# Kernel tuning notes

Hardware: AMD Instinct MI355X
Metric: run time of the kernel (lower is better)

The kernel has to match this reference:

```python
import jax, jax.numpy as jnp
import numpy as np

N_EMBD = 1024
N_HEAD = 16
MASK_FILL = -10000.0


def setup_inputs() -> dict:
    key = jax.random.key(0)
    ks = jax.random.split(key, 9)
    s = 1.0 / np.sqrt(N_EMBD)
    d = {"x": jax.random.normal(ks[0], (4, 2048, N_EMBD), dtype=jnp.float32)}
    for i, name in enumerate(["k", "q", "v", "p"]):
        d[f"W{name}"] = jax.random.uniform(ks[1 + 2 * i], (N_EMBD, N_EMBD), minval=-s, maxval=s, dtype=jnp.float32)
        d[f"b{name}"] = jax.random.uniform(ks[2 + 2 * i], (N_EMBD,), minval=-s, maxval=s, dtype=jnp.float32)
    return d


def reference(x, Wk, bk, Wq, bq, Wv, bv, Wp, bp):
    B, T, C = x.shape
    H, D = N_HEAD, C // N_HEAD
    # projections -> [B, H, T, D]
    def split_heads(y):
        return y.reshape(B, T, H, D).transpose(0, 2, 1, 3)
    k = split_heads(x @ Wk + bk)
    q = split_heads(x @ Wq + bq)
    v = split_heads(x @ Wv + bv)
    att = jnp.einsum("bhtd,bhsd->bhts", q, k) / jnp.sqrt(jnp.float32(D))
    causal = jnp.tril(jnp.ones((T, T), dtype=bool))  # [T, T]
    att = jnp.where(causal[None, None], att, MASK_FILL)
    att = jax.nn.softmax(att, axis=-1)
    y = jnp.einsum("bhts,bhsd->bhtd", att, v)
    y = y.transpose(0, 2, 1, 3).reshape(B, T, C)
    return y @ Wp + bp
```

## Files before the change

### kernel.cpp

```cpp
#include <hip/hip_runtime.h>
#include <hip/hip_bf16.h>

#define CDIM   1024
#define NHEADS 16
#define DHEAD  64
#define BATCH  4
#define TSEQ   2048
#define MROWS  (BATCH * TSEQ)
#define QSTR   3072
#define NEG_BIG (-1e30f)
#define MASKVAL (-3.0e38f)
#define SCALE_L2E 0.18033688011f
#define DEFER_TH 11.5416f

typedef __attribute__((ext_vector_type(8)))  short bf16x8;
typedef __attribute__((ext_vector_type(4)))  float f32x4;
typedef __attribute__((ext_vector_type(16))) float f32x16;

__device__ __forceinline__ unsigned short f2bf(float f) {
    __hip_bfloat16 h = __float2bfloat16(f);
    return *reinterpret_cast<unsigned short*>(&h);
}
__device__ __forceinline__ unsigned int cvtpk(float a, float b) {
    unsigned r;
    asm("v_cvt_pk_bf16_f32 %0, %1, %2" : "=v"(r) : "v"(a), "v"(b));
    return r;
}
__device__ __forceinline__ float ex2(float x) {
    float r; asm("v_exp_f32 %0, %1" : "=v"(r) : "v"(x)); return r;
}

__global__ __launch_bounds__(256)
void cvt_x_kernel(const float* __restrict__ in, unsigned short* __restrict__ out)
{
    size_t i = (size_t)blockIdx.x * 256 + threadIdx.x;
    const float4* p = reinterpret_cast<const float4*>(in) + i * 2;
    float4 a = p[0], b = p[1];
    uint4 o;
    o.x = (unsigned)f2bf(a.x) | ((unsigned)f2bf(a.y) << 16);
    o.y = (unsigned)f2bf(a.z) | ((unsigned)f2bf(a.w) << 16);
    o.z = (unsigned)f2bf(b.x) | ((unsigned)f2bf(b.y) << 16);
    o.w = (unsigned)f2bf(b.z) | ((unsigned)f2bf(b.w) << 16);
    *reinterpret_cast<uint4*>(out + i * 8) = o;
}

__global__ __launch_bounds__(256)
void wt_kernel(const float* __restrict__ W0, const float* __restrict__ W1,
               const float* __restrict__ W2, const float* __restrict__ W3,
               unsigned short* __restrict__ T0, unsigned short* __restrict__ T1,
               unsigned short* __restrict__ T2, unsigned short* __restrict__ T3)
{
    const float* W; unsigned short* T;
    switch (blockIdx.z) {
        case 0:  W = W0; T = T0; break;
        case 1:  W = W1; T = T1; break;
        case 2:  W = W2; T = T2; break;
        default: W = W3; T = T3; break;
    }
    __shared__ float tile[32][33];
    const int t = threadIdx.x;
    const int r = t >> 3;
    const int c4 = (t & 7) * 4;
    const int n0 = blockIdx.x * 32, k0 = blockIdx.y * 32;
    float4 v = *reinterpret_cast<const float4*>(&W[(size_t)(k0 + r) * CDIM + n0 + c4]);
    tile[r][c4 + 0] = v.x; tile[r][c4 + 1] = v.y;
    tile[r][c4 + 2] = v.z; tile[r][c4 + 3] = v.w;
    __syncthreads();
    uint2 o;
    o.x = (unsigned)f2bf(tile[c4 + 0][r]) | ((unsigned)f2bf(tile[c4 + 1][r]) << 16);
    o.y = (unsigned)f2bf(tile[c4 + 2][r]) | ((unsigned)f2bf(tile[c4 + 3][r]) << 16);
    *reinterpret_cast<uint2*>(&T[(size_t)(n0 + r) * CDIM + k0 + c4]) = o;
}

__global__ __launch_bounds__(256)
void pack_bias(const float* __restrict__ bq, const float* __restrict__ bk,
               const float* __restrict__ bv, float* __restrict__ o)
{
    int i = blockIdx.x * 256 + threadIdx.x;
    float v = (i < 1024) ? bq[i] : (i < 2048 ? bk[i - 1024] : bv[i - 2048]);
    o[i] = v;
}


#define GBAR8  asm volatile("s_barrier" ::: "memory")
#define LGKM0  asm volatile("s_waitcnt lgkmcnt(0)" ::: "memory")
#define VMC0   asm volatile("s_waitcnt vmcnt(0)" ::: "memory")

#define STAGE8(bufp, off, srcp) do { \
    __builtin_amdgcn_global_load_lds( \
        (const __attribute__((address_space(1))) void*)(srcp), \
        (__attribute__((address_space(3))) void*)((bufp) + (off) + wv * 1024), 16, 0, 0); \
    __builtin_amdgcn_global_load_lds( \
        (const __attribute__((address_space(1))) void*)((srcp) + 65536), \
        (__attribute__((address_space(3))) void*)((bufp) + (off) + 8192 + wv * 1024), 16, 0, 0); \
} while (0)

#define LDA_ALL(Ab) do { \
    _Pragma("unroll") for (int m_ = 0; m_ < 4; ++m_) { \
        const int rl_ = wr * 64 + m_ * 16 + lj; \
        _Pragma("unroll") for (int k_ = 0; k_ < 2; ++k_) \
            af[m_][k_] = *reinterpret_cast<const bf16x8*>( \
                (Ab) + rl_ * 128 + (((k_ * 4 + lg) ^ (lj & 7)) * 16)); \
    } } while (0)

#define LDB_PAIR(Bb, pairi) do { \
    _Pragma("unroll") for (int n_ = 0; n_ < 2; ++n_) { \
        const int rl_ = wc * 64 + ((pairi) * 2 + n_) * 16 + lj; \
        _Pragma("unroll") for (int k_ = 0; k_ < 2; ++k_) \
            bfr[n_][k_] = *reinterpret_cast<const bf16x8*>( \
                (Bb) + rl_ * 128 + (((k_ * 4 + lg) ^ (lj & 7)) * 16)); \
    } } while (0)

#define MM_PAIR(npair) do { \
    __builtin_amdgcn_s_setprio(1); \
    _Pragma("unroll") for (int m_ = 0; m_ < 4; ++m_) \
        _Pragma("unroll") for (int n_ = 0; n_ < 2; ++n_) \
            _Pragma("unroll") for (int k_ = 0; k_ < 2; ++k_) \
                acc[m_][(npair) * 2 + n_] = \
                    __builtin_amdgcn_mfma_f32_16x16x32_bf16( \
                        af[m_][k_], bfr[n_][k_], acc[m_][(npair) * 2 + n_], 0, 0, 0); \
    __builtin_amdgcn_s_setprio(0); \
} while (0)

template<int BM, int BN, int OUTMODE>
__global__ __launch_bounds__(512)
void gemm_8ph2(const unsigned short* __restrict__ A,
               const unsigned short* __restrict__ BT,
               const float* __restrict__ bias,
               void* __restrict__ Cout, int N, int nScaled)
{
    constexpr int WN = BN / 64;
    constexpr bool A_SMALL = (BM == 128);
    constexpr int AOFF = 0;
    constexpr int BOFF = BM * 128;
    constexpr int SOFF   = A_SMALL ? AOFF : BOFF;
    constexpr int LLOOFF = A_SMALL ? BOFF : AOFF;
    constexpr int LHIOFF = LLOOFF + 16384;

    __shared__ __align__(16) char lds8[2][(BM + BN) * 128];
    const int tid = threadIdx.x;
    const int nbn = N / BN;
    const int bid = blockIdx.x;
    const int wg  = (bid & 7) * ((int)gridDim.x >> 3) + (bid >> 3);
    const int n0  = (wg % nbn) * BN;
    const int m0  = (wg / nbn) * BM;

    const int lane = tid & 63, wv = tid >> 6;
    const int wr = wv / WN, wc = wv % WN;
    const int lj = lane & 15, lg = lane >> 4;
    const int srow = tid >> 3;
    const int gsw  = 8 * ((tid & 7) ^ ((tid >> 3) & 7));

    char* buf0 = &lds8[0][0];
    char* buf1 = &lds8[1][0];

    const unsigned short* Sm  = A_SMALL ? A : BT;
    const int             sb  = A_SMALL ? m0 : n0;
    const unsigned short* Lm  = A_SMALL ? BT : A;
    const int             lb  = A_SMALL ? n0 : m0;
    const unsigned short* Ss  = Sm + (size_t)(sb + srow) * 1024 + gsw;
    const unsigned short* Llo = Lm + (size_t)(lb + srow) * 1024 + gsw;
    const unsigned short* Lhi = Lm + (size_t)(lb + 128 + srow) * 1024 + gsw;

    f32x4 acc[4][4];
    #pragma unroll
    for (int i = 0; i < 4; ++i)
        #pragma unroll
        for (int j = 0; j < 4; ++j) acc[i][j] = f32x4{0.f, 0.f, 0.f, 0.f};

    STAGE8(buf0, SOFF,   Ss);
    STAGE8(buf0, LLOOFF, Llo);
    STAGE8(buf0, LHIOFF, Lhi);
    VMC0; GBAR8;

    bf16x8 af[4][2], bfr[2][2];

    for (int it = 0; it < 8; ++it) {
        const int e = 2 * it, o = e + 1;
        const bool se = (e + 2) < 16;

        {
            char* Ab = buf0 + AOFF;
            char* Bb = buf0 + BOFF;
            LDA_ALL(Ab); LDB_PAIR(Bb, 0);
            STAGE8(buf1, SOFF,   Ss  + o * 64);
            STAGE8(buf1, LLOOFF, Llo + o * 64);
            GBAR8; LGKM0; MM_PAIR(0); GBAR8;
            LDB_PAIR(Bb, 1);
            STAGE8(buf1, LHIOFF, Lhi + o * 64);
            GBAR8; LGKM0; MM_PAIR(1);
            VMC0; GBAR8;
        }
        {
            char* Ab = buf1 + AOFF;
            char* Bb = buf1 + BOFF;
            LDA_ALL(Ab); LDB_PAIR(Bb, 0);
            if (se) STAGE8(buf0, SOFF, Ss + (e + 2) * 64);
            GBAR8; LGKM0; MM_PAIR(0); GBAR8;
            LDB_PAIR(Bb, 1);
            if (se) {
                STAGE8(buf0, LLOOFF, Llo + (e + 2) * 64);
                STAGE8(buf0, LHIOFF, Lhi + (e + 2) * 64);
            }
            GBAR8; LGKM0; MM_PAIR(1);
            VMC0; GBAR8;
        }
    }

    const float sc = (OUTMODE == 0 && n0 < nScaled) ? SCALE_L2E : 1.0f;
    float bcol[4];
    #pragma unroll
    for (int nr = 0; nr < 4; ++nr) bcol[nr] = bias[n0 + wc * 64 + nr * 16 + lj];

    #pragma unroll
    for (int mr = 0; mr < 4; ++mr) {
        #pragma unroll
        for (int r4 = 0; r4 < 4; ++r4) {
            const int row = m0 + wr * 64 + mr * 16 + lg * 4 + r4;
            #pragma unroll
            for (int nr = 0; nr < 4; ++nr) {
                const int col = n0 + wc * 64 + nr * 16 + lj;
                float v = (acc[mr][nr][r4] + bcol[nr]) * sc;
                if (OUTMODE == 0)
                    reinterpret_cast<unsigned short*>(Cout)[(size_t)row * N + col] = f2bf(v);
                else
                    reinterpret_cast<float*>(Cout)[(size_t)row * N + col] = v;
            }
        }
    }
}

#define PV_STEP(m, T, rb) { \
    unsigned int w01 = cvtpk(T[(rb)+0], T[(rb)+1]); \
    unsigned int w23 = cvtpk(T[(rb)+2], T[(rb)+3]); \
    unsigned int w45 = cvtpk(T[(rb)+4], T[(rb)+5]); \
    unsigned int w67 = cvtpk(T[(rb)+6], T[(rb)+7]); \
    asm("v_permlane32_swap_b32 %0, %1" : "+v"(w01), "+v"(w45)); \
    asm("v_permlane32_swap_b32 %0, %1" : "+v"(w23), "+v"(w67)); \
    union { unsigned int u[4]; bf16x8 v; } pa; \
    pa.u[0] = w01; pa.u[1] = w23; pa.u[2] = w45; pa.u[3] = w67; \
    const int voff = (32 * (m) + 16 * hi) ^ lqswz; \
    bf16x8 va = *reinterpret_cast<const bf16x8*>(VTB + lq * 128 + voff); \
    bf16x8 vb = *reinterpret_cast<const bf16x8*>(VTB + (lq + 32) * 128 + voff); \
    y0 = __builtin_amdgcn_mfma_f32_32x32x16_bf16(va, pa.v, y0, 0, 0, 0); \
    y1 = __builtin_amdgcn_mfma_f32_32x32x16_bf16(vb, pa.v, y1, 0, 0, 0); \
}

__global__ __launch_bounds__(256)
void attn_mfma6(const unsigned short* __restrict__ QKV, unsigned short* __restrict__ Yb)
{
    __shared__ unsigned short Ks[64 * 64];
    __shared__ unsigned short VTs[64 * 64];
    __shared__ unsigned short Ysc[4][32 * 72];

    const int tid = threadIdx.x, lane = tid & 63, wid = tid >> 6;
    const int lq = lane & 31, hi = lane >> 5;
    const int lqswz = (lq & 7) << 4;

    const int id  = blockIdx.x;
    const int kk  = id >> 3;
    const int hb  = (id & 7) + 8 * (kk >> 3);
    const int pair = kk & 7;
    const int h = hb & 15, bz = hb >> 4;

    const size_t rowbase = (size_t)bz * TSEQ;
    const int hq = h * DHEAD, hk = 1024 + h * DHEAD, hv = 2048 + h * DHEAD;
    char* KsB = (char*)Ks;
    char* VTB = (char*)VTs;

    const int krow = tid >> 3;
    const int kswz = ((tid & 7) * 16) ^ ((krow & 7) << 4);
    const int vk2  = 2 * (tid & 31);
    const int vdg  = (tid >> 5) * 8;
    const int vkb  = vk2 * 2;

    for (int iter = 0; iter < 2; ++iter) {
        const int qtile = iter ? (15 - pair) : pair;
        const int q0 = qtile * 128;
        const int wq = q0 + wid * 32;

        bf16x8 qf[4];
        {
            const unsigned short* qp = QKV + (rowbase + wq + lq) * QSTR + hq + hi * 8;
            #pragma unroll
            for (int s = 0; s < 4; ++s)
                qf[s] = *reinterpret_cast<const bf16x8*>(qp + s * 16);
        }
        f32x16 y0, y1;
        #pragma unroll
        for (int r = 0; r < 16; ++r) { y0[r] = 0.f; y1[r] = 0.f; }
        float mrow = NEG_BIG, lrow = 0.f;

        const int ktend = 2 * qtile + 2;

        uint4 kr0, kr1, vr0, vr1;
        {
            const unsigned short* kp = QKV + (rowbase + krow) * QSTR + hk + (tid & 7) * 8;
            kr0 = *reinterpret_cast<const uint4*>(kp);
            kr1 = *reinterpret_cast<const uint4*>(kp + 32 * QSTR);
            const unsigned short* vp = QKV + (rowbase + vk2) * QSTR + hv + vdg;
            vr0 = *reinterpret_cast<const uint4*>(vp);
            vr1 = *reinterpret_cast<const uint4*>(vp + QSTR);
        }

        for (int kt = 0; kt < ktend; ++kt) {
            __syncthreads();
            *reinterpret_cast<uint4*>(KsB + krow * 128 + kswz) = kr0;
            *reinterpret_cast<uint4*>(KsB + (krow + 32) * 128 + kswz) = kr1;
            {
                unsigned pe, po;
                pe = __builtin_amdgcn_perm(vr1.x, vr0.x, 0x05040100u);
                po = __builtin_amdgcn_perm(vr1.x, vr0.x, 0x07060302u);
                *reinterpret_cast<unsigned*>(VTB + (vdg + 0) * 128 + (vkb ^ 0x00)) = pe;
                *reinterpret_cast<unsigned*>(VTB + (vdg + 1) * 128 + (vkb ^ 0x10)) = po;
                pe = __builtin_amdgcn_perm(vr1.y, vr0.y, 0x05040100u);
                po = __builtin_amdgcn_perm(vr1.y, vr0.y, 0x07060302u);
                *reinterpret_cast<unsigned*>(VTB + (vdg + 2) * 128 + (vkb ^ 0x20)) = pe;
                *reinterpret_cast<unsigned*>(VTB + (vdg + 3) * 128 + (vkb ^ 0x30)) = po;
                pe = __builtin_amdgcn_perm(vr1.z, vr0.z, 0x05040100u);
                po = __builtin_amdgcn_perm(vr1.z, vr0.z, 0x07060302u);
                *reinterpret_cast<unsigned*>(VTB + (vdg + 4) * 128 + (vkb ^ 0x40)) = pe;
                *reinterpret_cast<unsigned*>(VTB + (vdg + 5) * 128 + (vkb ^ 0x50)) = po;
                pe = __builtin_amdgcn_perm(vr1.w, vr0.w, 0x05040100u);
                po = __builtin_amdgcn_perm(vr1.w, vr0.w, 0x07060302u);
                *reinterpret_cast<unsigned*>(VTB + (vdg + 6) * 128 + (vkb ^ 0x60)) = pe;
                *reinterpret_cast<unsigned*>(VTB + (vdg + 7) * 128 + (vkb ^ 0x70)) = po;
            }
            __syncthreads();

            if (kt + 1 < ktend) {
                const unsigned short* kp = QKV + (rowbase + (kt + 1) * 64 + krow) * QSTR + hk + (tid & 7) * 8;
                kr0 = *reinterpret_cast<const uint4*>(kp);
                kr1 = *reinterpret_cast<const uint4*>(kp + 32 * QSTR);
                const unsigned short* vp = QKV + (rowbase + (kt + 1) * 64 + vk2) * QSTR + hv + vdg;
                vr0 = *reinterpret_cast<const uint4*>(vp);
                vr1 = *reinterpret_cast<const uint4*>(vp + QSTR);
            }

            if (kt * 64 > wq + 31) continue;

            f32x16 s0, s1;
            #pragma unroll
            for (int r = 0; r < 16; ++r) { s0[r] = 0.f; s1[r] = 0.f; }
            #pragma unroll
            for (int s = 0; s < 4; ++s) {
                const int off = (s * 32 + hi * 16) ^ lqswz;
                bf16x8 k0 = *reinterpret_cast<const bf16x8*>(KsB + lq * 128 + off);
                bf16x8 k1 = *reinterpret_cast<const bf16x8*>(KsB + (lq + 32) * 128 + off);
                s0 = __builtin_amdgcn_mfma_f32_32x32x16_bf16(k0, qf[s], s0, 0, 0, 0);
                s1 = __builtin_amdgcn_mfma_f32_32x32x16_bf16(k1, qf[s], s1, 0, 0, 0);
            }

            const bool diag = (kt * 64 + 63) > wq;
            if (diag) {
                const int q_own = wq + lq;
                #pragma unroll
                for (int r = 0; r < 16; ++r) {
                    const int kl = kt * 64 + (r & 3) + 8 * (r >> 2) + 4 * hi;
                    if (kl > q_own) s0[r] = MASKVAL;
                    if (kl + 32 > q_own) s1[r] = MASKVAL;
                }
            }

            float t8[8];
            #pragma unroll
            for (int r = 0; r < 8; ++r)
                t8[r] = fmaxf(fmaxf(s0[r], s0[r + 8]), fmaxf(s1[r], s1[r + 8]));
            #pragma unroll
            for (int r = 0; r < 4; ++r) t8[r] = fmaxf(t8[r], t8[r + 4]);
            float pm = fmaxf(fmaxf(t8[0], t8[1]), fmaxf(t8[2], t8[3]));
            pm = fmaxf(pm, __shfl_xor(pm, 32));

            if (__any(pm > mrow + DEFER_TH)) {
                const float mnew = fmaxf(mrow, pm);
                const float alpha = ex2(mrow - mnew);
                #pragma unroll
                for (int r = 0; r < 16; ++r) { y0[r] *= alpha; y1[r] *= alpha; }
                lrow *= alpha;
                mrow = mnew;
            }
            #pragma unroll
            for (int r = 0; r < 16; ++r) {
                s0[r] = ex2(s0[r] - mrow);
                s1[r] = ex2(s1[r] - mrow);
            }
            float a8[8];
            #pragma unroll
            for (int r = 0; r < 8; ++r) a8[r] = (s0[r] + s0[r + 8]) + (s1[r] + s1[r + 8]);
            #pragma unroll
            for (int r = 0; r < 4; ++r) a8[r] += a8[r + 4];
            float sum = (a8[0] + a8[1]) + (a8[2] + a8[3]);
            sum += __shfl_xor(sum, 32);
            lrow += sum;

            PV_STEP(0, s0, 0)
            PV_STEP(1, s0, 8)
            PV_STEP(2, s1, 0)
            PV_STEP(3, s1, 8)
        }

        {
            const float inv = 1.f / lrow;
            char* ysb = (char*)&Ysc[wid][0];
            #pragma unroll
            for (int t = 0; t < 8; ++t) {
                const int dl = ((2 * t) & 3) + 8 * (t >> 1) + 4 * hi;
                unsigned int wa = cvtpk(y0[2 * t] * inv, y0[2 * t + 1] * inv);
                unsigned int wb = cvtpk(y1[2 * t] * inv, y1[2 * t + 1] * inv);
                *reinterpret_cast<unsigned int*>(ysb + lq * 144 + dl * 2) = wa;
                *reinterpret_cast<unsigned int*>(ysb + lq * 144 + (dl + 32) * 2) = wb;
            }
            #pragma unroll
            for (int u = 0; u < 4; ++u) {
                const int rr = lane >> 1, ch = (lane & 1) + 2 * u;
                uint4 val = *reinterpret_cast<const uint4*>(ysb + rr * 144 + ch * 16);
                *reinterpret_cast<uint4*>(Yb + (rowbase + q0 + wid * 32 + rr) * CDIM + h * DHEAD + ch * 8) = val;
            }
        }
    }
}

extern "C" void kernel_launch(void* const* d_in, const int* in_sizes, int n_in,
                              void* d_out, int out_size, void* d_ws, size_t ws_size,
                              hipStream_t stream)
{
    const float* x  = (const float*)d_in[0];
    const float* Wk = (const float*)d_in[1];
    const float* bk = (const float*)d_in[2];
    const float* Wq = (const float*)d_in[3];
    const float* bq = (const float*)d_in[4];
    const float* Wv = (const float*)d_in[5];
    const float* bv = (const float*)d_in[6];
    const float* Wp = (const float*)d_in[7];
    const float* bp = (const float*)d_in[8];

    const size_t xe = (size_t)MROWS * CDIM;
    const size_t we = (size_t)CDIM * CDIM;
    unsigned short* xb    = (unsigned short*)d_ws;
    unsigned short* wqkvt = xb + xe;
    unsigned short* wpt   = wqkvt + 3 * we;
    unsigned short* qkv   = wpt + we;
    unsigned short* ab    = qkv + (size_t)MROWS * QSTR;
    float*          bias3 = (float*)(ab + xe);

    cvt_x_kernel<<<(int)(xe / 8 / 256), 256, 0, stream>>>(x, xb);
    wt_kernel<<<dim3(32, 32, 4), 256, 0, stream>>>(
        Wq, Wk, Wv, Wp, wqkvt, wqkvt + we, wqkvt + 2 * we, wpt);
    pack_bias<<<12, 256, 0, stream>>>(bq, bk, bv, bias3);

    gemm_8ph2<128, 256, 0><<<768, 512, 0, stream>>>(xb, wqkvt, bias3, qkv,
                                                    QSTR, 1024);

    attn_mfma6<<<512, 256, 0, stream>>>(qkv, ab);

    gemm_8ph2<256, 128, 1><<<256, 512, 0, stream>>>(ab, wpt, bp, d_out,
                                                    CDIM, 0);
}
```

Baseline: 169.1 us.

## Triple-buffer GEMM LDS staging to prefetch two k-tiles ahead

Replaces the double-buffered LDS pipeline in both projection GEMMs with a three-buffer rotation. Two k-tiles are prefetched, and each iteration waits only until the older tile's loads finish (vmcnt(6)), not until all outstanding loads complete. This is meant to hide global-to-LDS load latency behind MFMA work. LDS use grows by half, to 144KB per block, which may cut occupancy and relies on the vmcnt count matching the six global_load_lds issued per stage.

```diff
diff --git a/kernel.cpp b/kernel.cpp
--- a/kernel.cpp
+++ b/kernel.cpp
@@ -84,6 +84,7 @@
 
 #define GBAR8  asm volatile("s_barrier" ::: "memory")
 #define LGKM0  asm volatile("s_waitcnt lgkmcnt(0)" ::: "memory")
+#define VMC6   asm volatile("s_waitcnt vmcnt(6)" ::: "memory")
 #define VMC0   asm volatile("s_waitcnt vmcnt(0)" ::: "memory")
 
 #define STAGE8(bufp, off, srcp) do { \
@@ -124,7 +125,7 @@
 
 template<int BM, int BN, int OUTMODE>
 __global__ __launch_bounds__(512)
-void gemm_8ph2(const unsigned short* __restrict__ A,
+void gemm_8ph3(const unsigned short* __restrict__ A,
                const unsigned short* __restrict__ BT,
                const float* __restrict__ bias,
                void* __restrict__ Cout, int N, int nScaled)
@@ -136,8 +137,9 @@
     constexpr int SOFF   = A_SMALL ? AOFF : BOFF;
     constexpr int LLOOFF = A_SMALL ? BOFF : AOFF;
     constexpr int LHIOFF = LLOOFF + 16384;
-
-    __shared__ __align__(16) char lds8[2][(BM + BN) * 128];
+    constexpr int BUFSZ  = (BM + BN) * 128;
+
+    __shared__ __align__(16) char lds8[3 * BUFSZ];
     const int tid = threadIdx.x;
     const int nbn = N / BN;
     const int bid = blockIdx.x;
@@ -150,9 +152,6 @@
     const int lj = lane & 15, lg = lane >> 4;
     const int srow = tid >> 3;
     const int gsw  = 8 * ((tid & 7) ^ ((tid >> 3) & 7));
-
-    char* buf0 = &lds8[0][0];
-    char* buf1 = &lds8[1][0];
 
     const unsigned short* Sm  = A_SMALL ? A : BT;
     const int             sb  = A_SMALL ? m0 : n0;
@@ -168,43 +167,38 @@
         #pragma unroll
         for (int j = 0; j < 4; ++j) acc[i][j] = f32x4{0.f, 0.f, 0.f, 0.f};
 
-    STAGE8(buf0, SOFF,   Ss);
-    STAGE8(buf0, LLOOFF, Llo);
-    STAGE8(buf0, LHIOFF, Lhi);
-    VMC0; GBAR8;
+    char* bufA = &lds8[0];
+    char* bufB = &lds8[BUFSZ];
+    char* bufC = &lds8[2 * BUFSZ];
+
+    STAGE8(bufA, SOFF,   Ss);
+    STAGE8(bufA, LLOOFF, Llo);
+    STAGE8(bufA, LHIOFF, Lhi);
+    STAGE8(bufB, SOFF,   Ss  + 64);
+    STAGE8(bufB, LLOOFF, Llo + 64);
+    STAGE8(bufB, LHIOFF, Lhi + 64);
+    VMC6; GBAR8;
 
     bf16x8 af[4][2], bfr[2][2];
 
-    for (int it = 0; it < 8; ++it) {
-        const int e = 2 * it, o = e + 1;
-        const bool se = (e + 2) < 16;
-
-        {
-            char* Ab = buf0 + AOFF;
-            char* Bb = buf0 + BOFF;
-            LDA_ALL(Ab); LDB_PAIR(Bb, 0);
-            STAGE8(buf1, SOFF,   Ss  + o * 64);
-            STAGE8(buf1, LLOOFF, Llo + o * 64);
-            GBAR8; LGKM0; MM_PAIR(0); GBAR8;
-            LDB_PAIR(Bb, 1);
-            STAGE8(buf1, LHIOFF, Lhi + o * 64);
-            GBAR8; LGKM0; MM_PAIR(1);
-            VMC0; GBAR8;
-        }
-        {
-            char* Ab = buf1 + AOFF;
-            char* Bb = buf1 + BOFF;
-            LDA_ALL(Ab); LDB_PAIR(Bb, 0);
-            if (se) STAGE8(buf0, SOFF, Ss + (e + 2) * 64);
-            GBAR8; LGKM0; MM_PAIR(0); GBAR8;
-            LDB_PAIR(Bb, 1);
-            if (se) {
-                STAGE8(buf0, LLOOFF, Llo + (e + 2) * 64);
-                STAGE8(buf0, LHIOFF, Lhi + (e + 2) * 64);
-            }
-            GBAR8; LGKM0; MM_PAIR(1);
-            VMC0; GBAR8;
-        }
+    for (int t = 0; t < 16; ++t) {
+        const bool st = (t + 2) < 16;
+        const int  t2 = (t + 2) * 64;
+
+        LDA_ALL(bufA + AOFF); LDB_PAIR(bufA + BOFF, 0);
+        if (st) {
+            STAGE8(bufC, SOFF,   Ss  + t2);
+            STAGE8(bufC, LLOOFF, Llo + t2);
+        }
+        GBAR8; LGKM0; MM_PAIR(0); GBAR8;
+
+        LDB_PAIR(bufA + BOFF, 1);
+        if (st) STAGE8(bufC, LHIOFF, Lhi + t2);
+        GBAR8; LGKM0; MM_PAIR(1);
+        if (st) { VMC6; } else { VMC0; }
+        GBAR8;
+
+        char* tmp = bufA; bufA = bufB; bufB = bufC; bufC = tmp;
     }
 
     const float sc = (OUTMODE == 0 && n0 < nScaled) ? SCALE_L2E : 1.0f;
@@ -448,11 +442,11 @@
         Wq, Wk, Wv, Wp, wqkvt, wqkvt + we, wqkvt + 2 * we, wpt);
     pack_bias<<<12, 256, 0, stream>>>(bq, bk, bv, bias3);
 
-    gemm_8ph2<128, 256, 0><<<768, 512, 0, stream>>>(xb, wqkvt, bias3, qkv,
+    gemm_8ph3<128, 256, 0><<<768, 512, 0, stream>>>(xb, wqkvt, bias3, qkv,
                                                     QSTR, 1024);
 
     attn_mfma6<<<512, 256, 0, stream>>>(qkv, ab);
 
-    gemm_8ph2<256, 128, 1><<<256, 512, 0, stream>>>(ab, wpt, bp, d_out,
+    gemm_8ph3<256, 128, 1><<<256, 512, 0, stream>>>(ab, wpt, bp, d_out,
                                                     CDIM, 0);
 }
```

Measured after the change: 166.7 us. No clear change (-1.4%).
